# Performance work log

Measured on AMD Instinct MI355X. Metric: run time of the kernel, lower is better.

The kernel has to match this reference:

```python
import jax, jax.numpy as jnp
import numpy as np

NUM_GROUP = 256   # npoint for FPS
GROUP_SIZE = 32   # k nearest neighbors per center


def setup_inputs() -> dict:
    key = jax.random.key(0)
    xyz = jax.random.normal(key, (32, 8192, 3), dtype=jnp.float32)  # (B,N,3)
    return {"xyz": xyz}


def _farthest_point_sample(xyz, npoint):
    # xyz: (B,N,3) -> indices (B,npoint). Deterministic start at index 0
    # (torch version uses randint; math of the iteration is identical).
    B, N, _ = xyz.shape
    init_dist = jnp.full((B, N), 1e10, dtype=xyz.dtype)
    init_far = jnp.zeros((B,), dtype=jnp.int32)

    def step(carry, _):
        distance, farthest = carry
        centroid = jnp.take_along_axis(xyz, farthest[:, None, None], axis=1)  # (B,1,3)
        d = jnp.sum((xyz - centroid) ** 2, axis=-1)           # (B,N)
        distance = jnp.minimum(distance, d)                    # masked update
        new_far = jnp.argmax(distance, axis=-1).astype(jnp.int32)
        return (distance, new_far), farthest

    _, cents = jax.lax.scan(step, (init_dist, init_far), None, length=npoint)
    return cents.T  # (B,npoint)


def _square_distance(src, dst):
    # src:(B,G,3), dst:(B,N,3) -> (B,G,N)
    return (jnp.sum(src ** 2, axis=-1)[:, :, None]
            - 2.0 * jnp.einsum('bgc,bnc->bgn', src, dst)
            + jnp.sum(dst ** 2, axis=-1)[:, None, :])


def reference(xyz):
    fps_idx = _farthest_point_sample(xyz, NUM_GROUP)                 # (B,G)
    center = jax.vmap(lambda p, i: p[i])(xyz, fps_idx)               # (B,G,3)
    dists = _square_distance(center, xyz)                            # (B,G,N)
    _, group_idx = jax.lax.top_k(-dists, GROUP_SIZE)                 # k smallest dists
    grouped = jax.vmap(lambda p, i: p[i])(xyz, group_idx)            # (B,G,K,3)
    group_feature = grouped.mean(axis=2)                             # (B,G,3)
    return (center, group_feature)
```

## Files before the change

kernel.cpp:

```cpp
#include <hip/hip_runtime.h>
#include <stdint.h>

typedef unsigned long long u64;
typedef unsigned int u32;
typedef float v2f __attribute__((ext_vector_type(2)));

#define NB 32
#define NP 8192
#define NG 256
#define NK 32

__device__ __forceinline__ float dist3(float dx, float dy, float dz) {
    return __fadd_rn(__fadd_rn(__fmul_rn(dx, dx), __fmul_rn(dy, dy)), __fmul_rn(dz, dz));
}

#define DPP_STEP(v, ctrl, rmask) __builtin_amdgcn_update_dpp((int)(v), (int)(v), (ctrl), (rmask), 0xf, false)

__device__ __forceinline__ u32 wave_max_u32(u32 v) {
    u32 o;
    o = (u32)DPP_STEP(v, 0x111, 0xf); v = (o > v) ? o : v;
    o = (u32)DPP_STEP(v, 0x112, 0xf); v = (o > v) ? o : v;
    o = (u32)DPP_STEP(v, 0x114, 0xf); v = (o > v) ? o : v;
    o = (u32)DPP_STEP(v, 0x118, 0xf); v = (o > v) ? o : v;
    o = (u32)DPP_STEP(v, 0x142, 0xa); v = (o > v) ? o : v;
    o = (u32)DPP_STEP(v, 0x143, 0xc); v = (o > v) ? o : v;
    return (u32)__builtin_amdgcn_readlane((int)v, 63);
}

__device__ __forceinline__ u32 wave_min_u32(u32 v) {
    u32 o;
    o = (u32)DPP_STEP(v, 0x111, 0xf); v = (o < v) ? o : v;
    o = (u32)DPP_STEP(v, 0x112, 0xf); v = (o < v) ? o : v;
    o = (u32)DPP_STEP(v, 0x114, 0xf); v = (o < v) ? o : v;
    o = (u32)DPP_STEP(v, 0x118, 0xf); v = (o < v) ? o : v;
    o = (u32)DPP_STEP(v, 0x142, 0xa); v = (o < v) ? o : v;
    o = (u32)DPP_STEP(v, 0x143, 0xc); v = (o < v) ? o : v;
    return (u32)__builtin_amdgcn_readlane((int)v, 63);
}

__global__ __launch_bounds__(512, 2) void fps_kernel(const float* __restrict__ xyz,
                                                     float* __restrict__ out)
{
    #pragma clang fp contract(off)
    const int b = blockIdx.x;
    const int t = threadIdx.x;
    const int wid = t >> 6, lane = t & 63;

    __shared__ u64 wavekey[2][8];

    const float* base = xyz + (size_t)b * NP * 3;

    v2f px[8], py[8], pz[8], dist[8];
    {
        const float4* src = reinterpret_cast<const float4*>(base) + t * 12;
        float4 f[12];
        #pragma unroll
        for (int i = 0; i < 12; ++i) f[i] = src[i];
        float fl[48];
        #pragma unroll
        for (int i = 0; i < 12; ++i) {
            fl[4*i] = f[i].x; fl[4*i+1] = f[i].y; fl[4*i+2] = f[i].z; fl[4*i+3] = f[i].w;
        }
        #pragma unroll
        for (int j = 0; j < 8; ++j) {
            px[j] = (v2f){fl[6*j+0], fl[6*j+3]};
            py[j] = (v2f){fl[6*j+1], fl[6*j+4]};
            pz[j] = (v2f){fl[6*j+2], fl[6*j+5]};
            dist[j] = (v2f){1e10f, 1e10f};
        }
    }

    float cx, cy, cz;
    {
        float4 f0 = *reinterpret_cast<const float4*>(base);
        cx = f0.x; cy = f0.y; cz = f0.z;
        if (t == 0) {
            float* o = out + (size_t)b * NG * 3;
            o[0] = cx; o[1] = cy; o[2] = cz;
        }
    }

    for (int g = 0; g < NG - 1; ++g) {
        const v2f cvx = (v2f){cx, cx};
        const v2f cvy = (v2f){cy, cy};
        const v2f cvz = (v2f){cz, cz};
        float bestd = -1.0f;
        u32 bestj = 0;
        #pragma unroll
        for (int j = 0; j < 8; ++j) {
            v2f dx = px[j] - cvx;
            v2f dy = py[j] - cvy;
            v2f dz = pz[j] - cvz;
            v2f qx = dx * dx;
            v2f qy = dy * dy;
            v2f qz = dz * dz;
            v2f s  = (qx + qy) + qz;
            float d0 = fminf(dist[j].x, s.x);
            float d1 = fminf(dist[j].y, s.y);
            dist[j].x = d0;
            dist[j].y = d1;
            bool g0 = d0 > bestd;
            bestd = g0 ? d0 : bestd;
            bestj = g0 ? (u32)(2*j) : bestj;
            bool g1 = d1 > bestd;
            bestd = g1 ? d1 : bestd;
            bestj = g1 ? (u32)(2*j+1) : bestj;
        }
        u32 hi = __float_as_uint(bestd);
        u32 lo = (u32)(NP - 1 - (t * 16 + (int)bestj));
        u32 mh = wave_max_u32(hi);
        u32 cl = (hi == mh) ? lo : 0u;
        u32 ml = wave_max_u32(cl);
        if (lane == 0) wavekey[g & 1][wid] = ((u64)mh << 32) | (u64)ml;
        __syncthreads();

        u64 wk = wavekey[g & 1][0];
        #pragma unroll
        for (int w = 1; w < 8; ++w) {
            u64 o = wavekey[g & 1][w];
            wk = (o > wk) ? o : wk;
        }
        const int widx = NP - 1 - (int)(u32)(wk & 0xFFFFFFFFull);
        const float* cp = base + (size_t)widx * 3;
        cx = cp[0]; cy = cp[1]; cz = cp[2];
        if (t == 0) {
            float* o = out + ((size_t)b * NG + g + 1) * 3;
            o[0] = cx; o[1] = cy; o[2] = cz;
        }
    }
}

__device__ __forceinline__ void insert4(u64 pk, u64& t0, u64& t1, u64& t2, u64& t3) {
    if (pk < t3) {
        t3 = pk;
        if (t3 < t2) { u64 tmp = t2; t2 = t3; t3 = tmp; }
        if (t2 < t1) { u64 tmp = t1; t1 = t2; t2 = tmp; }
        if (t1 < t0) { u64 tmp = t0; t0 = t1; t1 = tmp; }
    }
}

__device__ __forceinline__ void scan_top4(const float4* __restrict__ gsrc,
                                          float* __restrict__ buf0,
                                          float* __restrict__ buf1,
                                          float cx, float cy, float cz, float s2,
                                          u64 L, bool useL, int lane,
                                          u64& t0, u64& t1, u64& t2, u64& t3)
{
    #pragma clang fp contract(off)
    t0 = t1 = t2 = t3 = ~0ull;

    {
        float4 a0 = gsrc[lane], a1 = gsrc[64 + lane], a2 = gsrc[128 + lane];
        float4* w0 = reinterpret_cast<float4*>(buf0);
        w0[lane] = a0; w0[64 + lane] = a1; w0[128 + lane] = a2;
    }
    float4 r0 = gsrc[192 + lane], r1 = gsrc[256 + lane], r2 = gsrc[320 + lane];

    for (int c = 0; c < 32; ++c) {
        float* cur = (c & 1) ? buf1 : buf0;
        float* nxt = (c & 1) ? buf0 : buf1;
        if (c < 31) {
            float4* wn = reinterpret_cast<float4*>(nxt);
            wn[lane] = r0; wn[64 + lane] = r1; wn[128 + lane] = r2;
        }
        if (c < 30) {
            const float4* gn = gsrc + (size_t)(c + 2) * 192;
            r0 = gn[lane]; r1 = gn[64 + lane]; r2 = gn[128 + lane];
        }
        #pragma unroll
        for (int k = 0; k < 4; ++k) {
            const int p = k * 64 + lane;
            const float* q = cur + 3 * p;
            float nx = q[0], ny = q[1], nz = q[2];
            float dotv = __fadd_rn(__fadd_rn(__fmul_rn(cx,nx), __fmul_rn(cy,ny)), __fmul_rn(cz,nz));
            float n2   = dist3(nx, ny, nz);
            float d    = __fadd_rn(__fsub_rn(s2, __fmul_rn(2.0f, dotv)), n2);
            u32 u  = __float_as_uint(d);
            u32 kk = u ^ (u32)(((int)u >> 31) | 0x80000000);
            int idx = c * 256 + p;
            u64 pk = ((u64)kk << 32) | (u64)(u32)idx;
            if (!useL || pk > L) insert4(pk, t0, t1, t2, t3);
        }
    }
}

__global__ __launch_bounds__(256) void knn_kernel(const float* __restrict__ xyz,
                                                  float* __restrict__ out)
{
    __shared__ float ldsbuf[4][2][768];

    const int t    = threadIdx.x;
    const int lane = t & 63;
    const int wid  = t >> 6;
    const int task = blockIdx.x * 4 + wid;
    const int b    = task >> 8;
    const int g    = task & 255;

    const float* cptr = out + ((size_t)b * NG + g) * 3;
    const float cx = cptr[0], cy = cptr[1], cz = cptr[2];
    const float s2 = dist3(cx, cy, cz);

    const float4* gsrc = reinterpret_cast<const float4*>(xyz + (size_t)b * NP * 3);
    float* buf0 = &ldsbuf[wid][0][0];
    float* buf1 = &ldsbuf[wid][1][0];

    u64 t0, t1, t2, t3;
    scan_top4(gsrc, buf0, buf1, cx, cy, cz, s2, 0ull, false, lane, t0, t1, t2, t3);
    int cnt = 4;
    u64 L = 0;
    u32 myWin = 0;

    for (int round = 0; round < NK; ++round) {
        if (__ballot(cnt == 0) != 0ull) {
            scan_top4(gsrc, buf0, buf1, cx, cy, cz, s2, L, L != 0ull, lane, t0, t1, t2, t3);
            cnt = 4;
        }
        u32 hi0 = (u32)(t0 >> 32);
        u32 lo0 = (u32)(t0 & 0xFFFFFFFFull);
        u32 mh = wave_min_u32(hi0);
        u32 cl = (hi0 == mh) ? lo0 : 0xFFFFFFFFu;
        u32 ml = wave_min_u32(cl);
        u64 w  = ((u64)mh << 32) | (u64)ml;
        if (t0 == w) {
            L = w;
            t0 = t1; t1 = t2; t2 = t3; t3 = ~0ull;
            --cnt;
        }
        if (lane == round) myWin = ml;
    }

    float sx = 0.f, sy = 0.f, sz = 0.f;
    if (lane < NK) {
        const float* p = xyz + ((size_t)b * NP + myWin) * 3;
        sx = p[0]; sy = p[1]; sz = p[2];
    }
    #pragma unroll
    for (int m = 32; m >= 1; m >>= 1) {
        sx += __shfl_xor(sx, m, 64);
        sy += __shfl_xor(sy, m, 64);
        sz += __shfl_xor(sz, m, 64);
    }
    if (lane == 0) {
        float* o = out + (size_t)NB * NG * 3 + ((size_t)b * NG + g) * 3;
        const float inv = 1.0f / 32.0f;
        o[0] = sx * inv; o[1] = sy * inv; o[2] = sz * inv;
    }
}

extern "C" void kernel_launch(void* const* d_in, const int* in_sizes, int n_in,
                              void* d_out, int out_size, void* d_ws, size_t ws_size,
                              hipStream_t stream)
{
    const float* xyz = (const float*)d_in[0];
    float* out = (float*)d_out;

    hipLaunchKernelGGL(fps_kernel, dim3(NB), dim3(512), 0, stream, xyz, out);

    const int tasks  = NB * NG;
    const int blocks = tasks / 4;
    hipLaunchKernelGGL(knn_kernel, dim3(blocks), dim3(256), 0, stream, xyz, out);
}
```

Measured before the change: 378.3 us.

## Stage FPS points in LDS, broadcast winner coords, read KNN points directly

The FPS kernel now keeps its points in shared memory in SoA layout and reloads them each iteration instead of holding them in registers. The winning lane writes its coordinates to shared memory, so the next centroid no longer needs a dependent global load. The KNN scan drops its per-wave LDS double buffer and reads float3 points straight from global memory with software prefetch. The aim is lower register pressure and a shorter serial FPS critical path, at the cost of extra LDS traffic per iteration and relying on cache for the KNN loads.

Result: slower. 491.9 us (+30.0%).

```diff
diff --git a/kernel.cpp b/kernel.cpp
--- a/kernel.cpp
+++ b/kernel.cpp
@@ -38,19 +38,22 @@
     return (u32)__builtin_amdgcn_readlane((int)v, 63);
 }
 
+#define F4C(v, c) ((c) == 0 ? (v).x : ((c) == 1 ? (v).y : ((c) == 2 ? (v).z : (v).w)))
+
 __global__ __launch_bounds__(512, 2) void fps_kernel(const float* __restrict__ xyz,
                                                      float* __restrict__ out)
 {
     #pragma clang fp contract(off)
+    __shared__ float4 pbuf[512 * 13];
+    __shared__ u64 wkey[2][8];
+    __shared__ float wcoord[2][8][4];
+
     const int b = blockIdx.x;
     const int t = threadIdx.x;
-    const int wid = t >> 6, lane = t & 63;
-
-    __shared__ u64 wavekey[2][8];
+    const int wid = t >> 6;
 
     const float* base = xyz + (size_t)b * NP * 3;
 
-    v2f px[8], py[8], pz[8], dist[8];
     {
         const float4* src = reinterpret_cast<const float4*>(base) + t * 12;
         float4 f[12];
@@ -61,14 +64,21 @@
         for (int i = 0; i < 12; ++i) {
             fl[4*i] = f[i].x; fl[4*i+1] = f[i].y; fl[4*i+2] = f[i].z; fl[4*i+3] = f[i].w;
         }
-        #pragma unroll
-        for (int j = 0; j < 8; ++j) {
-            px[j] = (v2f){fl[6*j+0], fl[6*j+3]};
-            py[j] = (v2f){fl[6*j+1], fl[6*j+4]};
-            pz[j] = (v2f){fl[6*j+2], fl[6*j+5]};
-            dist[j] = (v2f){1e10f, 1e10f};
-        }
-    }
+        float4* myb = pbuf + t * 13;
+        #pragma unroll
+        for (int s = 0; s < 4; ++s)
+            myb[s] = (float4){fl[3*(4*s+0)], fl[3*(4*s+1)], fl[3*(4*s+2)], fl[3*(4*s+3)]};
+        #pragma unroll
+        for (int s = 0; s < 4; ++s)
+            myb[4+s] = (float4){fl[3*(4*s+0)+1], fl[3*(4*s+1)+1], fl[3*(4*s+2)+1], fl[3*(4*s+3)+1]};
+        #pragma unroll
+        for (int s = 0; s < 4; ++s)
+            myb[8+s] = (float4){fl[3*(4*s+0)+2], fl[3*(4*s+1)+2], fl[3*(4*s+2)+2], fl[3*(4*s+3)+2]};
+    }
+
+    v2f dist[8];
+    #pragma unroll
+    for (int j = 0; j < 8; ++j) dist[j] = (v2f){1e10f, 1e10f};
 
     float cx, cy, cz;
     {
@@ -79,8 +89,18 @@
             o[0] = cx; o[1] = cy; o[2] = cz;
         }
     }
+    __syncthreads();
+
+    u32 mof = (u32)(t * 13 * 16);
 
     for (int g = 0; g < NG - 1; ++g) {
+        asm volatile("" : "+v"(mof));
+        const float4* myb = reinterpret_cast<const float4*>(
+            reinterpret_cast<const char*>(pbuf) + mof);
+        float4 S[12];
+        #pragma unroll
+        for (int s = 0; s < 12; ++s) S[s] = myb[s];
+
         const v2f cvx = (v2f){cx, cx};
         const v2f cvy = (v2f){cy, cy};
         const v2f cvz = (v2f){cz, cz};
@@ -88,17 +108,16 @@
         u32 bestj = 0;
         #pragma unroll
         for (int j = 0; j < 8; ++j) {
-            v2f dx = px[j] - cvx;
-            v2f dy = py[j] - cvy;
-            v2f dz = pz[j] - cvz;
-            v2f qx = dx * dx;
-            v2f qy = dy * dy;
-            v2f qz = dz * dz;
-            v2f s  = (qx + qy) + qz;
-            float d0 = fminf(dist[j].x, s.x);
-            float d1 = fminf(dist[j].y, s.y);
-            dist[j].x = d0;
-            dist[j].y = d1;
+            v2f pxp = (j & 1) ? (v2f){S[j>>1].z,     S[j>>1].w}     : (v2f){S[j>>1].x,     S[j>>1].y};
+            v2f pyp = (j & 1) ? (v2f){S[4+(j>>1)].z, S[4+(j>>1)].w} : (v2f){S[4+(j>>1)].x, S[4+(j>>1)].y};
+            v2f pzp = (j & 1) ? (v2f){S[8+(j>>1)].z, S[8+(j>>1)].w} : (v2f){S[8+(j>>1)].x, S[8+(j>>1)].y};
+            v2f dx = pxp - cvx;
+            v2f dy = pyp - cvy;
+            v2f dz = pzp - cvz;
+            v2f q  = (dx * dx + dy * dy) + dz * dz;
+            float d0 = fminf(dist[j].x, q.x);
+            float d1 = fminf(dist[j].y, q.y);
+            dist[j].x = d0; dist[j].y = d1;
             bool g0 = d0 > bestd;
             bestd = g0 ? d0 : bestd;
             bestj = g0 ? (u32)(2*j) : bestj;
@@ -111,18 +130,35 @@
         u32 mh = wave_max_u32(hi);
         u32 cl = (hi == mh) ? lo : 0u;
         u32 ml = wave_max_u32(cl);
-        if (lane == 0) wavekey[g & 1][wid] = ((u64)mh << 32) | (u64)ml;
+        if (hi == mh && lo == ml) {
+            float wx = 0.f, wy = 0.f, wz = 0.f;
+            #pragma unroll
+            for (int p = 0; p < 16; ++p) {
+                if (bestj == (u32)p) {
+                    wx = F4C(S[p >> 2],     p & 3);
+                    wy = F4C(S[4 + (p>>2)], p & 3);
+                    wz = F4C(S[8 + (p>>2)], p & 3);
+                }
+            }
+            wkey[g & 1][wid] = ((u64)mh << 32) | (u64)ml;
+            wcoord[g & 1][wid][0] = wx;
+            wcoord[g & 1][wid][1] = wy;
+            wcoord[g & 1][wid][2] = wz;
+        }
         __syncthreads();
 
-        u64 wk = wavekey[g & 1][0];
+        u64 wk = wkey[g & 1][0];
+        int wsel = 0;
         #pragma unroll
         for (int w = 1; w < 8; ++w) {
-            u64 o = wavekey[g & 1][w];
-            wk = (o > wk) ? o : wk;
-        }
-        const int widx = NP - 1 - (int)(u32)(wk & 0xFFFFFFFFull);
-        const float* cp = base + (size_t)widx * 3;
-        cx = cp[0]; cy = cp[1]; cz = cp[2];
+            u64 o = wkey[g & 1][w];
+            bool gt = o > wk;
+            wk = gt ? o : wk;
+            wsel = gt ? w : wsel;
+        }
+        cx = wcoord[g & 1][wsel][0];
+        cy = wcoord[g & 1][wsel][1];
+        cz = wcoord[g & 1][wsel][2];
         if (t == 0) {
             float* o = out + ((size_t)b * NG + g + 1) * 3;
             o[0] = cx; o[1] = cy; o[2] = cz;
@@ -139,56 +175,59 @@
     }
 }
 
-__device__ __forceinline__ void scan_top4(const float4* __restrict__ gsrc,
-                                          float* __restrict__ buf0,
-                                          float* __restrict__ buf1,
+__device__ __forceinline__ float3 ld3(const float* p) {
+    return *reinterpret_cast<const float3*>(p);
+}
+
+#define KPROC(P, IDX) { \
+    float nx = (P).x, ny = (P).y, nz = (P).z; \
+    float dotv = __fadd_rn(__fadd_rn(__fmul_rn(cx,nx), __fmul_rn(cy,ny)), __fmul_rn(cz,nz)); \
+    float n2   = dist3(nx, ny, nz); \
+    float d    = __fadd_rn(__fsub_rn(s2, __fmul_rn(2.0f, dotv)), n2); \
+    u32 u  = __float_as_uint(d); \
+    u32 kk = u ^ (u32)(((int)u >> 31) | 0x80000000); \
+    u64 pk = ((u64)kk << 32) | (u64)(u32)(IDX); \
+    if (!useL || pk > L) insert4(pk, t0, t1, t2, t3); }
+
+__device__ __forceinline__ void scan_top4(const float* __restrict__ pts,
                                           float cx, float cy, float cz, float s2,
                                           u64 L, bool useL, int lane,
                                           u64& t0, u64& t1, u64& t2, u64& t3)
 {
     #pragma clang fp contract(off)
     t0 = t1 = t2 = t3 = ~0ull;
-
-    {
-        float4 a0 = gsrc[lane], a1 = gsrc[64 + lane], a2 = gsrc[128 + lane];
-        float4* w0 = reinterpret_cast<float4*>(buf0);
-        w0[lane] = a0; w0[64 + lane] = a1; w0[128 + lane] = a2;
-    }
-    float4 r0 = gsrc[192 + lane], r1 = gsrc[256 + lane], r2 = gsrc[320 + lane];
-
-    for (int c = 0; c < 32; ++c) {
-        float* cur = (c & 1) ? buf1 : buf0;
-        float* nxt = (c & 1) ? buf0 : buf1;
-        if (c < 31) {
-            float4* wn = reinterpret_cast<float4*>(nxt);
-            wn[lane] = r0; wn[64 + lane] = r1; wn[128 + lane] = r2;
-        }
-        if (c < 30) {
-            const float4* gn = gsrc + (size_t)(c + 2) * 192;
-            r0 = gn[lane]; r1 = gn[64 + lane]; r2 = gn[128 + lane];
-        }
-        #pragma unroll
-        for (int k = 0; k < 4; ++k) {
-            const int p = k * 64 + lane;
-            const float* q = cur + 3 * p;
-            float nx = q[0], ny = q[1], nz = q[2];
-            float dotv = __fadd_rn(__fadd_rn(__fmul_rn(cx,nx), __fmul_rn(cy,ny)), __fmul_rn(cz,nz));
-            float n2   = dist3(nx, ny, nz);
-            float d    = __fadd_rn(__fsub_rn(s2, __fmul_rn(2.0f, dotv)), n2);
-            u32 u  = __float_as_uint(d);
-            u32 kk = u ^ (u32)(((int)u >> 31) | 0x80000000);
-            int idx = c * 256 + p;
-            u64 pk = ((u64)kk << 32) | (u64)(u32)idx;
-            if (!useL || pk > L) insert4(pk, t0, t1, t2, t3);
-        }
+    const float* lp = pts + lane * 3;
+
+    float3 a0, a1, a2, a3, b0, b1, b2, b3;
+    a0 = ld3(lp);       a1 = ld3(lp + 192);
+    a2 = ld3(lp + 384); a3 = ld3(lp + 576);
+
+    for (int c = 0; c < 32; c += 2) {
+        const float* q1 = lp + (size_t)(c + 1) * 768;
+        b0 = ld3(q1);       b1 = ld3(q1 + 192);
+        b2 = ld3(q1 + 384); b3 = ld3(q1 + 576);
+
+        KPROC(a0, c*256 +       lane);
+        KPROC(a1, c*256 +  64 + lane);
+        KPROC(a2, c*256 + 128 + lane);
+        KPROC(a3, c*256 + 192 + lane);
+
+        if (c + 2 < 32) {
+            const float* q2 = lp + (size_t)(c + 2) * 768;
+            a0 = ld3(q2);       a1 = ld3(q2 + 192);
+            a2 = ld3(q2 + 384); a3 = ld3(q2 + 576);
+        }
+
+        KPROC(b0, (c+1)*256 +       lane);
+        KPROC(b1, (c+1)*256 +  64 + lane);
+        KPROC(b2, (c+1)*256 + 128 + lane);
+        KPROC(b3, (c+1)*256 + 192 + lane);
     }
 }
 
 __global__ __launch_bounds__(256) void knn_kernel(const float* __restrict__ xyz,
                                                   float* __restrict__ out)
 {
-    __shared__ float ldsbuf[4][2][768];
-
     const int t    = threadIdx.x;
     const int lane = t & 63;
     const int wid  = t >> 6;
@@ -200,19 +239,17 @@
     const float cx = cptr[0], cy = cptr[1], cz = cptr[2];
     const float s2 = dist3(cx, cy, cz);
 
-    const float4* gsrc = reinterpret_cast<const float4*>(xyz + (size_t)b * NP * 3);
-    float* buf0 = &ldsbuf[wid][0][0];
-    float* buf1 = &ldsbuf[wid][1][0];
+    const float* pts = xyz + (size_t)b * NP * 3;
 
     u64 t0, t1, t2, t3;
-    scan_top4(gsrc, buf0, buf1, cx, cy, cz, s2, 0ull, false, lane, t0, t1, t2, t3);
+    scan_top4(pts, cx, cy, cz, s2, 0ull, false, lane, t0, t1, t2, t3);
     int cnt = 4;
     u64 L = 0;
     u32 myWin = 0;
 
     for (int round = 0; round < NK; ++round) {
         if (__ballot(cnt == 0) != 0ull) {
-            scan_top4(gsrc, buf0, buf1, cx, cy, cz, s2, L, L != 0ull, lane, t0, t1, t2, t3);
+            scan_top4(pts, cx, cy, cz, s2, L, L != 0ull, lane, t0, t1, t2, t3);
             cnt = 4;
         }
         u32 hi0 = (u32)(t0 >> 32);
```
